# Kernel tuning notes

Measured on AMD Instinct MI355X. Metric: run time of the kernel, lower is better.

Reference implementation:

```python
import jax, jax.numpy as jnp
import numpy as np

N = 100000   # nodes
DEG = 16     # in-degree per node
E = N * DEG  # edges
D = 64       # embedding_dim


def mobius_addition(x, y, c):
    xy = jnp.sum(x * y, axis=-1, keepdims=True)
    x2 = jnp.sum(x * x, axis=-1, keepdims=True)
    y2 = jnp.sum(y * y, axis=-1, keepdims=True)
    num = (1 + 2 * c * xy + c * y2) * x + (1 - c * x2) * y
    den = 1 + 2 * c * xy + c * c * x2 * y2
    return num / den


def exp_map(x, v, c):
    vn = jnp.linalg.norm(v, axis=-1, keepdims=True)
    sc = jnp.sqrt(c)
    second = jnp.tanh(sc * vn / 2) * v / (sc * vn)
    return mobius_addition(x, second, c)


def log_map(x, y, c):
    add = mobius_addition(-x, y, c)
    an = jnp.linalg.norm(add, axis=-1, keepdims=True)
    sc = jnp.sqrt(c)
    return 2 / sc * jnp.arctanh(sc * an) * add / an


def setup_inputs() -> dict:
    key = jax.random.key(0)
    ks = jax.random.split(key, 6)
    # scale so points are well inside the Poincare ball (atanh domain)
    x = jax.random.normal(ks[0], (N, D), jnp.float32) * 0.01
    src = jax.random.randint(ks[1], (E,), 0, N, dtype=jnp.int32)
    # every node gets exactly DEG in-edges -> no isolated nodes (avoids 0/0 in exp_map)
    dst = jnp.repeat(jnp.arange(N, dtype=jnp.int32), DEG)
    s = 1.0 / np.sqrt(D)
    Wq = jax.random.normal(ks[2], (D, D), jnp.float32) * s
    Wk = jax.random.normal(ks[3], (D, D), jnp.float32) * s
    Wv = jax.random.normal(ks[4], (D, D), jnp.float32) * s
    bq = jnp.zeros((D,), jnp.float32)
    bk = jnp.zeros((D,), jnp.float32)
    bv = jnp.zeros((D,), jnp.float32)
    curvature = jnp.ones((1,), jnp.float32)
    return {"x": x, "curvature": curvature, "Wq": Wq, "bq": bq, "Wk": Wk,
            "bk": bk, "Wv": Wv, "bv": bv, "src": src, "dst": dst}


def reference(x, curvature, Wq, bq, Wk, bk, Wv, bv, src, dst):
    c = curvature  # (1,), broadcasts against (N,1) keepdim norms
    n = x.shape[0]
    origin = jnp.zeros_like(x[:1])  # (1, D)
    tangent = log_map(origin, x, c)  # (N, D)
    # torch nn.Linear: y = x @ W.T + b
    q = tangent @ Wq.T + bq
    k = tangent @ Wk.T + bk
    v = tangent @ Wv.T + bv
    scale = jnp.asarray(x.shape[-1] ** 0.5, x.dtype)
    # per-edge score: <k[src], q[dst]> / sqrt(d)
    scores = jnp.einsum('ed,ed->e', k[src], q[dst]) / scale  # (E,)
    # segment (per-dst) softmax over incoming edges
    smax = jax.ops.segment_max(scores, dst, num_segments=n)
    ex = jnp.exp(scores - smax[dst])
    ssum = jax.ops.segment_sum(ex, dst, num_segments=n)
    alpha = ex / ssum[dst]  # (E,)
    # weighted scatter-sum of src values
    h = jax.ops.segment_sum(alpha[:, None] * v[src], dst, num_segments=n)  # (N, D)
    return exp_map(origin, h, c)
```

## Files before the change

kernel.cpp:

```cpp
#include <hip/hip_runtime.h>
#include <hip/hip_bf16.h>
#include <math.h>


typedef __attribute__((ext_vector_type(8))) short bf16x8;
typedef __attribute__((ext_vector_type(4))) float f32x4;
typedef __attribute__((ext_vector_type(2))) float f32x2;

static __device__ __forceinline__ short f2bf(float f) {
    union { __hip_bfloat16 h; short s; } u; u.h = __float2bfloat16(f); return u.s;
}
static __device__ __forceinline__ float bflo(unsigned u) {
    return __uint_as_float(u << 16);
}
static __device__ __forceinline__ float bfhi(unsigned u) {
    return __uint_as_float(u & 0xffff0000u);
}

#define UBCVT(F, SRC, IDX) asm("v_cvt_f32_ubyte" IDX " %0, %1" : "=v"(F) : "v"(SRC))

#define TSTRIDE 72
#define SQSTR   72
#define SKSTR   72
#define SVSTR   68

__global__ __launch_bounds__(256) void qkv_kernel(
    const float* __restrict__ x,
    const float* __restrict__ cur,
    const float* __restrict__ Wq, const float* __restrict__ bq,
    const float* __restrict__ Wk, const float* __restrict__ bk,
    const float* __restrict__ Wv, const float* __restrict__ bv,
    unsigned short* __restrict__ qb, unsigned char* __restrict__ kvl,
    float* __restrict__ vs, int N)
{
    __shared__ short tL[128 * TSTRIDE];
    __shared__ short sq[16 * SQSTR];
    __shared__ unsigned char sk[16 * SKSTR];
    __shared__ float svf[16 * SVSTR];
    const int tid = threadIdx.x;
    const int w = tid >> 6, lane = tid & 63;
    const int blockBase = blockIdx.x * 128;
    const float sc = __builtin_amdgcn_sqrtf(cur[0]);

    const int rr = lane >> 2, p = lane & 3;
    #pragma unroll
    for (int it = 0; it < 2; ++it) {
        const int rloc = w * 32 + it * 16 + rr;
        int row = blockBase + rloc; if (row >= N) row = N - 1;
        const float4* xr = (const float4*)(x + (size_t)row * 64 + p * 16);
        float4 x0 = xr[0], x1 = xr[1], x2 = xr[2], x3 = xr[3];
        float pn = x0.x*x0.x + x0.y*x0.y + x0.z*x0.z + x0.w*x0.w
                 + x1.x*x1.x + x1.y*x1.y + x1.z*x1.z + x1.w*x1.w
                 + x2.x*x2.x + x2.y*x2.y + x2.z*x2.z + x2.w*x2.w
                 + x3.x*x3.x + x3.y*x3.y + x3.z*x3.z + x3.w*x3.w;
        pn += __shfl_xor(pn, 1, 64);
        pn += __shfl_xor(pn, 2, 64);
        float z = sc * __builtin_amdgcn_sqrtf(pn);
        float ts = (z > 1e-12f)
            ? (__logf((1.0f + z) * __builtin_amdgcn_rcpf(1.0f - z))
               * __builtin_amdgcn_rcpf(z))
            : 2.0f;
        bf16x8 t0, t1;
        t0[0]=f2bf(ts*x0.x); t0[1]=f2bf(ts*x0.y); t0[2]=f2bf(ts*x0.z); t0[3]=f2bf(ts*x0.w);
        t0[4]=f2bf(ts*x1.x); t0[5]=f2bf(ts*x1.y); t0[6]=f2bf(ts*x1.z); t0[7]=f2bf(ts*x1.w);
        t1[0]=f2bf(ts*x2.x); t1[1]=f2bf(ts*x2.y); t1[2]=f2bf(ts*x2.z); t1[3]=f2bf(ts*x2.w);
        t1[4]=f2bf(ts*x3.x); t1[5]=f2bf(ts*x3.y); t1[6]=f2bf(ts*x3.z); t1[7]=f2bf(ts*x3.w);
        bf16x8* dst = (bf16x8*)&tL[rloc * TSTRIDE + p * 16];
        dst[0] = t0; dst[1] = t1;
    }
    __syncthreads();

    const int n16 = lane & 15, quad = lane >> 4;
    bf16x8 Bf[3][2];
    float bias[3];
    int matv[3], col0v[3];
    #pragma unroll
    for (int tt = 0; tt < 3; ++tt) {
        const int tile = w * 3 + tt;
        const int mat = tile >> 2;
        const int col0 = (tile & 3) * 16;
        matv[tt] = mat; col0v[tt] = col0;
        const float* Wm = (mat == 0) ? Wq : (mat == 1) ? Wk : Wv;
        const float* bm = (mat == 0) ? bq : (mat == 1) ? bk : bv;
        const float* srcp = Wm + (col0 + n16) * 64 + quad * 8;
        #pragma unroll
        for (int h = 0; h < 2; ++h) {
            float4 a = *(const float4*)(srcp + h * 32);
            float4 b = *(const float4*)(srcp + h * 32 + 4);
            bf16x8 f;
            f[0]=f2bf(a.x); f[1]=f2bf(a.y); f[2]=f2bf(a.z); f[3]=f2bf(a.w);
            f[4]=f2bf(b.x); f[5]=f2bf(b.y); f[6]=f2bf(b.z); f[7]=f2bf(b.w);
            Bf[tt][h] = f;
        }
        bias[tt] = bm[col0 + n16];
    }

    const int crow = tid >> 4;
    const int c8   = tid & 15;

    for (int nt = 0; nt < 8; ++nt) {
        const short* ar = &tL[(nt * 16 + n16) * TSTRIDE + quad * 8];
        bf16x8 A0 = *(const bf16x8*)ar;
        bf16x8 A1 = *(const bf16x8*)(ar + 32);
        #pragma unroll
        for (int tt = 0; tt < 3; ++tt) {
            f32x4 acc = { bias[tt], bias[tt], bias[tt], bias[tt] };
            acc = __builtin_amdgcn_mfma_f32_16x16x32_bf16(A0, Bf[tt][0], acc, 0, 0, 0);
            acc = __builtin_amdgcn_mfma_f32_16x16x32_bf16(A1, Bf[tt][1], acc, 0, 0, 0);
            const int mat = matv[tt], col0 = col0v[tt];
            #pragma unroll
            for (int r4 = 0; r4 < 4; ++r4) {
                const int rl = quad * 4 + r4;
                const int c  = col0 + n16;
                if (mat == 0) {
                    sq[rl * SQSTR + c] = f2bf(acc[r4]);
                } else if (mat == 1) {
                    int pk = __builtin_amdgcn_cvt_pk_fp8_f32(acc[r4], acc[r4], 0, false);
                    sk[rl * SKSTR + c] = (unsigned char)(pk & 0xff);
                } else {
                    svf[rl * SVSTR + c] = acc[r4];
                }
            }
        }
        __syncthreads();

        const int node = blockBase + nt * 16 + crow;
        {
            f32x4 v4 = *(const f32x4*)&svf[crow * SVSTR + c8 * 4];
            float m = fmaxf(fmaxf(fabsf(v4[0]), fabsf(v4[1])),
                            fmaxf(fabsf(v4[2]), fabsf(v4[3])));
            m = fmaxf(m, __shfl_xor(m, 1, 64));
            m = fmaxf(m, __shfl_xor(m, 2, 64));
            m = fmaxf(m, __shfl_xor(m, 4, 64));
            m = fmaxf(m, __shfl_xor(m, 8, 64));
            float rm = fmaxf(m, 1e-20f);
            float inv = 127.0f * __builtin_amdgcn_rcpf(rm);
            float scale = rm * (1.0f / 127.0f);
            int i0 = __float2int_rn(v4[0] * inv) + 128;
            int i1 = __float2int_rn(v4[1] * inv) + 128;
            int i2 = __float2int_rn(v4[2] * inv) + 128;
            int i3 = __float2int_rn(v4[3] * inv) + 128;
            unsigned pk = (unsigned)(i0 & 255) | ((unsigned)(i1 & 255) << 8)
                        | ((unsigned)(i2 & 255) << 16) | ((unsigned)(i3 & 255) << 24);
            if (node < N) {
                *(uint2*)(qb + (size_t)node * 64 + c8 * 4) =
                    *(const uint2*)&sq[crow * SQSTR + c8 * 4];
                *(unsigned*)(kvl + (size_t)node * 128 + c8 * 4) =
                    *(const unsigned*)&sk[crow * SKSTR + c8 * 4];
                *(unsigned*)(kvl + (size_t)node * 128 + 64 + c8 * 4) = pk;
                if (c8 == 0) vs[node] = scale;
            }
        }
        __syncthreads();
    }
}

__global__ __launch_bounds__(256) void attn_kernel(
    const unsigned short* __restrict__ qb, const unsigned char* __restrict__ kvl,
    const float* __restrict__ vs, const int* __restrict__ src,
    const float* __restrict__ cur,
    float* __restrict__ out, int N)
{
    __shared__ float aA[4][2][16];
    const int tid = threadIdx.x;
    const int w = tid >> 6, lane = tid & 63;
    const int wg = blockIdx.x * 4 + w;
    const int stride = gridDim.x * 8;

    const int j = lane >> 2, p = lane & 3;
    const int g = lane >> 4, m = lane & 15;
    const float c0 = cur[0];
    const float sc = __builtin_amdgcn_sqrtf(c0);
    const unsigned dimoff = (unsigned)(m << 2);

    int n0 = wg * 2;
    if (n0 >= N) return;

    int  sjA0 = src[n0 * 16 + j];
    int  sjA1 = src[n0 * 16 + 16 + j];
    int4 s4A0 = *(const int4*)(src + n0 * 16 + (g << 2));
    int4 s4A1 = *(const int4*)(src + n0 * 16 + 16 + (g << 2));

    while (true) {
        const int n1 = n0 + 1;
        const int nn = n0 + stride;
        const int sj0 = sjA0, sj1 = sjA1;
        const int4 s40 = s4A0, s41 = s4A1;

        const unsigned vo00 = ((unsigned)s40.x << 7) + dimoff;
        const unsigned vo01 = ((unsigned)s40.y << 7) + dimoff;
        const unsigned vo02 = ((unsigned)s40.z << 7) + dimoff;
        const unsigned vo03 = ((unsigned)s40.w << 7) + dimoff;
        const unsigned vr00 = *(const unsigned*)(kvl + 64 + vo00);
        const unsigned vr01 = *(const unsigned*)(kvl + 64 + vo01);
        const unsigned vr02 = *(const unsigned*)(kvl + 64 + vo02);
        const unsigned vr03 = *(const unsigned*)(kvl + 64 + vo03);
        const unsigned vo10 = ((unsigned)s41.x << 7) + dimoff;
        const unsigned vo11 = ((unsigned)s41.y << 7) + dimoff;
        const unsigned vo12 = ((unsigned)s41.z << 7) + dimoff;
        const unsigned vo13 = ((unsigned)s41.w << 7) + dimoff;
        const unsigned vr10 = *(const unsigned*)(kvl + 64 + vo10);
        const unsigned vr11 = *(const unsigned*)(kvl + 64 + vo11);
        const unsigned vr12 = *(const unsigned*)(kvl + 64 + vo12);
        const unsigned vr13 = *(const unsigned*)(kvl + 64 + vo13);

        const unsigned ko0 = ((unsigned)sj0 << 7) + (unsigned)(p << 4);
        const unsigned ko1 = ((unsigned)sj1 << 7) + (unsigned)(p << 4);
        const uint4 kd0 = *(const uint4*)(kvl + ko0);
        const uint4 kd1 = *(const uint4*)(kvl + ko1);
        const float sjs0 = vs[sj0];
        const float sjs1 = vs[sj1];

        const uint4* qp0 = (const uint4*)(qb + (size_t)n0 * 64 + (p << 4));
        const uint4 qa0 = qp0[0], qc0 = qp0[1];
        const uint4* qp1 = (const uint4*)(qb + (size_t)n1 * 64 + (p << 4));
        const uint4 qa1 = qp1[0], qc1 = qp1[1];

        int sjB0, sjB1; int4 s4B0, s4B1;
        const bool more = (nn < N);
        if (more) {
            sjB0 = src[nn * 16 + j];
            sjB1 = src[nn * 16 + 16 + j];
            s4B0 = *(const int4*)(src + nn * 16 + (g << 2));
            s4B1 = *(const int4*)(src + nn * 16 + 16 + (g << 2));
        }

        float acc0 = 0.f;
        {
            f32x2 k0 = __builtin_amdgcn_cvt_pk_f32_fp8(kd0.x, false);
            f32x2 k1 = __builtin_amdgcn_cvt_pk_f32_fp8(kd0.x, true);
            acc0 = fmaf(k0[0], bflo(qa0.x), acc0); acc0 = fmaf(k0[1], bfhi(qa0.x), acc0);
            acc0 = fmaf(k1[0], bflo(qa0.y), acc0); acc0 = fmaf(k1[1], bfhi(qa0.y), acc0);
            k0 = __builtin_amdgcn_cvt_pk_f32_fp8(kd0.y, false);
            k1 = __builtin_amdgcn_cvt_pk_f32_fp8(kd0.y, true);
            acc0 = fmaf(k0[0], bflo(qa0.z), acc0); acc0 = fmaf(k0[1], bfhi(qa0.z), acc0);
            acc0 = fmaf(k1[0], bflo(qa0.w), acc0); acc0 = fmaf(k1[1], bfhi(qa0.w), acc0);
            k0 = __builtin_amdgcn_cvt_pk_f32_fp8(kd0.z, false);
            k1 = __builtin_amdgcn_cvt_pk_f32_fp8(kd0.z, true);
            acc0 = fmaf(k0[0], bflo(qc0.x), acc0); acc0 = fmaf(k0[1], bfhi(qc0.x), acc0);
            acc0 = fmaf(k1[0], bflo(qc0.y), acc0); acc0 = fmaf(k1[1], bfhi(qc0.y), acc0);
            k0 = __builtin_amdgcn_cvt_pk_f32_fp8(kd0.w, false);
            k1 = __builtin_amdgcn_cvt_pk_f32_fp8(kd0.w, true);
            acc0 = fmaf(k0[0], bflo(qc0.z), acc0); acc0 = fmaf(k0[1], bfhi(qc0.z), acc0);
            acc0 = fmaf(k1[0], bflo(qc0.w), acc0); acc0 = fmaf(k1[1], bfhi(qc0.w), acc0);
        }
        acc0 += __shfl_xor(acc0, 1, 64);
        acc0 += __shfl_xor(acc0, 2, 64);
        float ex0 = __builtin_amdgcn_exp2f(acc0 * (0.125f * 1.44269504f));
        float ss0 = ex0;
        #pragma unroll
        for (int mm = 4; mm < 64; mm <<= 1) ss0 += __shfl_xor(ss0, mm, 64);
        float as0 = ex0 * sjs0 * __builtin_amdgcn_rcpf(ss0);
        if (p == 0) aA[w][0][j] = as0;

        float acc1 = 0.f;
        {
            f32x2 k0 = __builtin_amdgcn_cvt_pk_f32_fp8(kd1.x, false);
            f32x2 k1 = __builtin_amdgcn_cvt_pk_f32_fp8(kd1.x, true);
            acc1 = fmaf(k0[0], bflo(qa1.x), acc1); acc1 = fmaf(k0[1], bfhi(qa1.x), acc1);
            acc1 = fmaf(k1[0], bflo(qa1.y), acc1); acc1 = fmaf(k1[1], bfhi(qa1.y), acc1);
            k0 = __builtin_amdgcn_cvt_pk_f32_fp8(kd1.y, false);
            k1 = __builtin_amdgcn_cvt_pk_f32_fp8(kd1.y, true);
            acc1 = fmaf(k0[0], bflo(qa1.z), acc1); acc1 = fmaf(k0[1], bfhi(qa1.z), acc1);
            acc1 = fmaf(k1[0], bflo(qa1.w), acc1); acc1 = fmaf(k1[1], bfhi(qa1.w), acc1);
            k0 = __builtin_amdgcn_cvt_pk_f32_fp8(kd1.z, false);
            k1 = __builtin_amdgcn_cvt_pk_f32_fp8(kd1.z, true);
            acc1 = fmaf(k0[0], bflo(qc1.x), acc1); acc1 = fmaf(k0[1], bfhi(qc1.x), acc1);
            acc1 = fmaf(k1[0], bflo(qc1.y), acc1); acc1 = fmaf(k1[1], bfhi(qc1.y), acc1);
            k0 = __builtin_amdgcn_cvt_pk_f32_fp8(kd1.w, false);
            k1 = __builtin_amdgcn_cvt_pk_f32_fp8(kd1.w, true);
            acc1 = fmaf(k0[0], bflo(qc1.z), acc1); acc1 = fmaf(k0[1], bfhi(qc1.z), acc1);
            acc1 = fmaf(k1[0], bflo(qc1.w), acc1); acc1 = fmaf(k1[1], bfhi(qc1.w), acc1);
        }
        acc1 += __shfl_xor(acc1, 1, 64);
        acc1 += __shfl_xor(acc1, 2, 64);
        float ex1 = __builtin_amdgcn_exp2f(acc1 * (0.125f * 1.44269504f));
        float ss1 = ex1;
        #pragma unroll
        for (int mm = 4; mm < 64; mm <<= 1) ss1 += __shfl_xor(ss1, mm, 64);
        float as1 = ex1 * sjs1 * __builtin_amdgcn_rcpf(ss1);
        if (p == 0) aA[w][1][j] = as1;

        __builtin_amdgcn_wave_barrier();
        const float4 a40 = *(const float4*)&aA[w][0][g << 2];
        const float4 a41 = *(const float4*)&aA[w][1][g << 2];
        __builtin_amdgcn_wave_barrier();
        const float sa0 = (a40.x + a40.y) + (a40.z + a40.w);
        const float sa1 = (a41.x + a41.y) + (a41.z + a41.w);

        float h00 = 0.f, h01 = 0.f, h02 = 0.f, h03 = 0.f;
        float h10 = 0.f, h11 = 0.f, h12 = 0.f, h13 = 0.f;
        {
            float f0, f1, f2, f3;
            UBCVT(f0, vr00, "0"); UBCVT(f1, vr00, "1"); UBCVT(f2, vr00, "2"); UBCVT(f3, vr00, "3");
            h00 = fmaf(a40.x, f0, h00); h01 = fmaf(a40.x, f1, h01);
            h02 = fmaf(a40.x, f2, h02); h03 = fmaf(a40.x, f3, h03);
            UBCVT(f0, vr01, "0"); UBCVT(f1, vr01, "1"); UBCVT(f2, vr01, "2"); UBCVT(f3, vr01, "3");
            h00 = fmaf(a40.y, f0, h00); h01 = fmaf(a40.y, f1, h01);
            h02 = fmaf(a40.y, f2, h02); h03 = fmaf(a40.y, f3, h03);
            UBCVT(f0, vr02, "0"); UBCVT(f1, vr02, "1"); UBCVT(f2, vr02, "2"); UBCVT(f3, vr02, "3");
            h00 = fmaf(a40.z, f0, h00); h01 = fmaf(a40.z, f1, h01);
            h02 = fmaf(a40.z, f2, h02); h03 = fmaf(a40.z, f3, h03);
            UBCVT(f0, vr03, "0"); UBCVT(f1, vr03, "1"); UBCVT(f2, vr03, "2"); UBCVT(f3, vr03, "3");
            h00 = fmaf(a40.w, f0, h00); h01 = fmaf(a40.w, f1, h01);
            h02 = fmaf(a40.w, f2, h02); h03 = fmaf(a40.w, f3, h03);

            UBCVT(f0, vr10, "0"); UBCVT(f1, vr10, "1"); UBCVT(f2, vr10, "2"); UBCVT(f3, vr10, "3");
            h10 = fmaf(a41.x, f0, h10); h11 = fmaf(a41.x, f1, h11);
            h12 = fmaf(a41.x, f2, h12); h13 = fmaf(a41.x, f3, h13);
            UBCVT(f0, vr11, "0"); UBCVT(f1, vr11, "1"); UBCVT(f2, vr11, "2"); UBCVT(f3, vr11, "3");
            h10 = fmaf(a41.y, f0, h10); h11 = fmaf(a41.y, f1, h11);
            h12 = fmaf(a41.y, f2, h12); h13 = fmaf(a41.y, f3, h13);
            UBCVT(f0, vr12, "0"); UBCVT(f1, vr12, "1"); UBCVT(f2, vr12, "2"); UBCVT(f3, vr12, "3");
            h10 = fmaf(a41.z, f0, h10); h11 = fmaf(a41.z, f1, h11);
            h12 = fmaf(a41.z, f2, h12); h13 = fmaf(a41.z, f3, h13);
            UBCVT(f0, vr13, "0"); UBCVT(f1, vr13, "1"); UBCVT(f2, vr13, "2"); UBCVT(f3, vr13, "3");
            h10 = fmaf(a41.w, f0, h10); h11 = fmaf(a41.w, f1, h11);
            h12 = fmaf(a41.w, f2, h12); h13 = fmaf(a41.w, f3, h13);
        }
        const float cr0 = 128.0f * sa0;
        const float cr1 = 128.0f * sa1;
        h00 -= cr0; h01 -= cr0; h02 -= cr0; h03 -= cr0;
        h10 -= cr1; h11 -= cr1; h12 -= cr1; h13 -= cr1;

        h00 += __shfl_xor(h00, 16, 64); h01 += __shfl_xor(h01, 16, 64);
        h02 += __shfl_xor(h02, 16, 64); h03 += __shfl_xor(h03, 16, 64);
        h10 += __shfl_xor(h10, 16, 64); h11 += __shfl_xor(h11, 16, 64);
        h12 += __shfl_xor(h12, 16, 64); h13 += __shfl_xor(h13, 16, 64);
        h00 += __shfl_xor(h00, 32, 64); h01 += __shfl_xor(h01, 32, 64);
        h02 += __shfl_xor(h02, 32, 64); h03 += __shfl_xor(h03, 32, 64);
        h10 += __shfl_xor(h10, 32, 64); h11 += __shfl_xor(h11, 32, 64);
        h12 += __shfl_xor(h12, 32, 64); h13 += __shfl_xor(h13, 32, 64);

        float n20 = h00*h00 + h01*h01 + h02*h02 + h03*h03;
        float n21 = h10*h10 + h11*h11 + h12*h12 + h13*h13;
        n20 += __shfl_xor(n20, 1, 64); n21 += __shfl_xor(n21, 1, 64);
        n20 += __shfl_xor(n20, 2, 64); n21 += __shfl_xor(n21, 2, 64);
        n20 += __shfl_xor(n20, 4, 64); n21 += __shfl_xor(n21, 4, 64);
        n20 += __shfl_xor(n20, 8, 64); n21 += __shfl_xor(n21, 8, 64);
        float z0 = sc * __builtin_amdgcn_sqrtf(n20);
        float z1 = sc * __builtin_amdgcn_sqrtf(n21);
        float e0 = __builtin_amdgcn_exp2f(z0 * 1.44269504f);
        float e1 = __builtin_amdgcn_exp2f(z1 * 1.44269504f);
        float sc0 = (z0 > 1e-12f)
            ? ((e0 - 1.0f) * __builtin_amdgcn_rcpf(z0 * (e0 + 1.0f))) : 0.5f;
        float sc1 = (z1 > 1e-12f)
            ? ((e1 - 1.0f) * __builtin_amdgcn_rcpf(z1 * (e1 + 1.0f))) : 0.5f;
        if (lane < 16) {
            float4 o0 = make_float4(sc0 * h00, sc0 * h01, sc0 * h02, sc0 * h03);
            float4 o1 = make_float4(sc1 * h10, sc1 * h11, sc1 * h12, sc1 * h13);
            *(float4*)(out + (size_t)n0 * 64 + (lane << 2)) = o0;
            *(float4*)(out + (size_t)n1 * 64 + (lane << 2)) = o1;
        }

        if (!more) break;
        n0 = nn;
        sjA0 = sjB0; sjA1 = sjB1; s4A0 = s4B0; s4A1 = s4B1;
    }
}

extern "C" void kernel_launch(void* const* d_in, const int* in_sizes, int n_in,
                              void* d_out, int out_size, void* d_ws, size_t ws_size,
                              hipStream_t stream)
{
    const float* x   = (const float*)d_in[0];
    const float* cur = (const float*)d_in[1];
    const float* Wq  = (const float*)d_in[2];
    const float* bq  = (const float*)d_in[3];
    const float* Wk  = (const float*)d_in[4];
    const float* bk  = (const float*)d_in[5];
    const float* Wv  = (const float*)d_in[6];
    const float* bv  = (const float*)d_in[7];
    const int* src = (const int*)d_in[8];

    const int N = in_sizes[0] / 64;

    unsigned short* qb  = (unsigned short*)d_ws;
    unsigned char*  kvl = (unsigned char*)(qb + (size_t)N * 64);
    float*          vsc = (float*)(kvl + (size_t)N * 128);

    const int blocks1 = (N + 127) / 128;
    int blocks2 = 2048;
    const int need = (N + 7) / 8;
    if (blocks2 > need) blocks2 = need;
    qkv_kernel<<<blocks1, 256, 0, stream>>>(x, cur, Wq, bq, Wk, bk, Wv, bv,
                                            qb, kvl, vsc, N);
    attn_kernel<<<blocks2, 256, 0, stream>>>(qb, kvl, vsc, src, cur,
                                             (float*)d_out, N);
}
```

Before: 154.5 us.

## Precompute bf16 weight fragments and double-buffer QKV staging to drop barriers

A new single-block kernel converts Wq/Wk/Wv to bf16 MFMA fragments and gathers the biases into workspace once. The QKV blocks then load these prepared fragments instead of each block converting the fp32 weights itself. The QKV kernel also now handles 64 rows per block instead of 128, which launches twice as many blocks. Its output staging buffers are double-buffered, so one __syncthreads per tile iteration can be removed. The cost is an extra kernel launch and a bit more workspace, and the likely bottleneck, the attention kernel, is unchanged.

```diff
diff --git a/kernel.cpp b/kernel.cpp
--- a/kernel.cpp
+++ b/kernel.cpp
@@ -24,28 +24,51 @@
 #define SKSTR   72
 #define SVSTR   68
 
+__global__ __launch_bounds__(768) void wprep_kernel(
+    const float* __restrict__ Wq, const float* __restrict__ bq,
+    const float* __restrict__ Wk, const float* __restrict__ bk,
+    const float* __restrict__ Wv, const float* __restrict__ bv,
+    unsigned short* __restrict__ wf, float* __restrict__ bfA)
+{
+    const int t = threadIdx.x;
+    const int tile = t >> 6, lane = t & 63;
+    const int n16 = lane & 15, quad = lane >> 4;
+    const int mat = tile >> 2, col0 = (tile & 3) * 16;
+    const float* Wm = (mat == 0) ? Wq : (mat == 1) ? Wk : Wv;
+    const float* bm = (mat == 0) ? bq : (mat == 1) ? bk : bv;
+    const float* srcp = Wm + (col0 + n16) * 64 + quad * 8;
+    unsigned short* dst = wf + ((size_t)tile * 64 + lane) * 16;
+    #pragma unroll
+    for (int h = 0; h < 2; ++h) {
+        float4 a = *(const float4*)(srcp + h * 32);
+        float4 b = *(const float4*)(srcp + h * 32 + 4);
+        bf16x8 f;
+        f[0]=f2bf(a.x); f[1]=f2bf(a.y); f[2]=f2bf(a.z); f[3]=f2bf(a.w);
+        f[4]=f2bf(b.x); f[5]=f2bf(b.y); f[6]=f2bf(b.z); f[7]=f2bf(b.w);
+        *(bf16x8*)(dst + h * 8) = f;
+    }
+    if (lane < 16) bfA[tile * 16 + lane] = bm[col0 + lane];
+}
+
 __global__ __launch_bounds__(256) void qkv_kernel(
     const float* __restrict__ x,
     const float* __restrict__ cur,
-    const float* __restrict__ Wq, const float* __restrict__ bq,
-    const float* __restrict__ Wk, const float* __restrict__ bk,
-    const float* __restrict__ Wv, const float* __restrict__ bv,
+    const unsigned short* __restrict__ wf, const float* __restrict__ bfA,
     unsigned short* __restrict__ qb, unsigned char* __restrict__ kvl,
     float* __restrict__ vs, int N)
 {
-    __shared__ short tL[128 * TSTRIDE];
-    __shared__ short sq[16 * SQSTR];
-    __shared__ unsigned char sk[16 * SKSTR];
-    __shared__ float svf[16 * SVSTR];
+    __shared__ short tL[64 * TSTRIDE];
+    __shared__ short sq[2][16 * SQSTR];
+    __shared__ unsigned char sk[2][16 * SKSTR];
+    __shared__ float svf[2][16 * SVSTR];
     const int tid = threadIdx.x;
     const int w = tid >> 6, lane = tid & 63;
-    const int blockBase = blockIdx.x * 128;
+    const int blockBase = blockIdx.x * 64;
     const float sc = __builtin_amdgcn_sqrtf(cur[0]);
 
     const int rr = lane >> 2, p = lane & 3;
-    #pragma unroll
-    for (int it = 0; it < 2; ++it) {
-        const int rloc = w * 32 + it * 16 + rr;
+    {
+        const int rloc = w * 16 + rr;
         int row = blockBase + rloc; if (row >= N) row = N - 1;
         const float4* xr = (const float4*)(x + (size_t)row * 64 + p * 16);
         float4 x0 = xr[0], x1 = xr[1], x2 = xr[2], x3 = xr[3];
@@ -68,7 +91,6 @@
         bf16x8* dst = (bf16x8*)&tL[rloc * TSTRIDE + p * 16];
         dst[0] = t0; dst[1] = t1;
     }
-    __syncthreads();
 
     const int n16 = lane & 15, quad = lane >> 4;
     bf16x8 Bf[3][2];
@@ -77,28 +99,21 @@
     #pragma unroll
     for (int tt = 0; tt < 3; ++tt) {
         const int tile = w * 3 + tt;
-        const int mat = tile >> 2;
-        const int col0 = (tile & 3) * 16;
-        matv[tt] = mat; col0v[tt] = col0;
-        const float* Wm = (mat == 0) ? Wq : (mat == 1) ? Wk : Wv;
-        const float* bm = (mat == 0) ? bq : (mat == 1) ? bk : bv;
-        const float* srcp = Wm + (col0 + n16) * 64 + quad * 8;
-        #pragma unroll
-        for (int h = 0; h < 2; ++h) {
-            float4 a = *(const float4*)(srcp + h * 32);
-            float4 b = *(const float4*)(srcp + h * 32 + 4);
-            bf16x8 f;
-            f[0]=f2bf(a.x); f[1]=f2bf(a.y); f[2]=f2bf(a.z); f[3]=f2bf(a.w);
-            f[4]=f2bf(b.x); f[5]=f2bf(b.y); f[6]=f2bf(b.z); f[7]=f2bf(b.w);
-            Bf[tt][h] = f;
-        }
-        bias[tt] = bm[col0 + n16];
+        matv[tt] = tile >> 2;
+        col0v[tt] = (tile & 3) * 16;
+        const uint4* wp = (const uint4*)(wf + ((size_t)tile * 64 + lane) * 16);
+        uint4 f0 = wp[0], f1 = wp[1];
+        Bf[tt][0] = *(bf16x8*)&f0;
+        Bf[tt][1] = *(bf16x8*)&f1;
+        bias[tt] = bfA[tile * 16 + n16];
     }
+    __syncthreads();
 
     const int crow = tid >> 4;
     const int c8   = tid & 15;
 
-    for (int nt = 0; nt < 8; ++nt) {
+    for (int nt = 0; nt < 4; ++nt) {
+        const int b = nt & 1;
         const short* ar = &tL[(nt * 16 + n16) * TSTRIDE + quad * 8];
         bf16x8 A0 = *(const bf16x8*)ar;
         bf16x8 A1 = *(const bf16x8*)(ar + 32);
@@ -113,12 +128,12 @@
                 const int rl = quad * 4 + r4;
                 const int c  = col0 + n16;
                 if (mat == 0) {
-                    sq[rl * SQSTR + c] = f2bf(acc[r4]);
+                    sq[b][rl * SQSTR + c] = f2bf(acc[r4]);
                 } else if (mat == 1) {
                     int pk = __builtin_amdgcn_cvt_pk_fp8_f32(acc[r4], acc[r4], 0, false);
-                    sk[rl * SKSTR + c] = (unsigned char)(pk & 0xff);
+                    sk[b][rl * SKSTR + c] = (unsigned char)(pk & 0xff);
                 } else {
-                    svf[rl * SVSTR + c] = acc[r4];
+                    svf[b][rl * SVSTR + c] = acc[r4];
                 }
             }
         }
@@ -126,7 +141,7 @@
 
         const int node = blockBase + nt * 16 + crow;
         {
-            f32x4 v4 = *(const f32x4*)&svf[crow * SVSTR + c8 * 4];
+            f32x4 v4 = *(const f32x4*)&svf[b][crow * SVSTR + c8 * 4];
             float m = fmaxf(fmaxf(fabsf(v4[0]), fabsf(v4[1])),
                             fmaxf(fabsf(v4[2]), fabsf(v4[3])));
             m = fmaxf(m, __shfl_xor(m, 1, 64));
@@ -144,14 +159,13 @@
                         | ((unsigned)(i2 & 255) << 16) | ((unsigned)(i3 & 255) << 24);
             if (node < N) {
                 *(uint2*)(qb + (size_t)node * 64 + c8 * 4) =
-                    *(const uint2*)&sq[crow * SQSTR + c8 * 4];
+                    *(const uint2*)&sq[b][crow * SQSTR + c8 * 4];
                 *(unsigned*)(kvl + (size_t)node * 128 + c8 * 4) =
-                    *(const unsigned*)&sk[crow * SKSTR + c8 * 4];
+                    *(const unsigned*)&sk[b][crow * SKSTR + c8 * 4];
                 *(unsigned*)(kvl + (size_t)node * 128 + 64 + c8 * 4) = pk;
                 if (c8 == 0) vs[node] = scale;
             }
         }
-        __syncthreads();
     }
 }
 
@@ -378,13 +392,15 @@
     unsigned short* qb  = (unsigned short*)d_ws;
     unsigned char*  kvl = (unsigned char*)(qb + (size_t)N * 64);
     float*          vsc = (float*)(kvl + (size_t)N * 128);
-
-    const int blocks1 = (N + 127) / 128;
+    unsigned short* wf  = (unsigned short*)(vsc + N);
+    float*          bfA = (float*)(wf + 12 * 64 * 16);
+
+    const int blocks1 = (N + 63) / 64;
     int blocks2 = 2048;
     const int need = (N + 7) / 8;
     if (blocks2 > need) blocks2 = need;
-    qkv_kernel<<<blocks1, 256, 0, stream>>>(x, cur, Wq, bq, Wk, bk, Wv, bv,
-                                            qb, kvl, vsc, N);
+    wprep_kernel<<<1, 768, 0, stream>>>(Wq, bq, Wk, bk, Wv, bv, wf, bfA);
+    qkv_kernel<<<blocks1, 256, 0, stream>>>(x, cur, wf, bfA, qb, kvl, vsc, N);
     attn_kernel<<<blocks2, 256, 0, stream>>>(qb, kvl, vsc, src, cur,
                                              (float*)d_out, N);
 }
```

Result: faster. 150.2 us (-2.8%).
